# Kernel optimization log

Hardware: AMD Instinct MI355X
Metric: run time of the kernel (lower is better)

The kernel has to match this reference:

```python
import jax, jax.numpy as jnp
import numpy as np
from jax import lax

NSITE, NCELL, BSZ = 101, 64, 1
D_MODEL, D_INNER, D_STATE, D_CONV, DT_RANK = 64, 128, 16, 4, 4
L = NSITE * NCELL


def setup_inputs() -> dict:
    key = jax.random.key(0)
    ks = jax.random.split(key, 16)
    f = lambda k, s, sc=0.05: jax.random.normal(k, s, jnp.float32) * sc
    return {
        "DNAinput": f(ks[0], (BSZ, L, 32), 1.0),
        "CpGinput": f(ks[1], (BSZ, L, 16), 1.0),
        "cellinput": f(ks[2], (BSZ, L, 16), 1.0),
        "pos": f(ks[3], (BSZ, L, D_MODEL), 1.0),
        "y_true": jax.random.uniform(ks[4], (64,), jnp.float32),
        "W_fcc": f(ks[5], (64, D_MODEL)),
        "b_fcc": jnp.zeros((D_MODEL,), jnp.float32),
        "W_in": f(ks[6], (D_MODEL, 2 * D_INNER)),
        "conv_w": f(ks[7], (D_INNER, D_CONV)),
        "conv_b": jnp.zeros((D_INNER,), jnp.float32),
        "W_xp": f(ks[8], (D_INNER, DT_RANK + 2 * D_STATE)),
        "W_dt": f(ks[9], (DT_RANK, D_INNER)),
        "b_dt": f(ks[10], (D_INNER,)),
        "A_log": jnp.log(jnp.broadcast_to(jnp.arange(1, D_STATE + 1, dtype=jnp.float32), (D_INNER, D_STATE))),
        "Dres": jnp.ones((D_INNER,), jnp.float32),
        "W_out": f(ks[11], (D_INNER, D_MODEL)),
        "ln_g": jnp.ones((D_MODEL,), jnp.float32),
        "ln_b": jnp.zeros((D_MODEL,), jnp.float32),
        "W_fc": f(ks[12], (D_MODEL, 1)),
        "b_fc": jnp.zeros((1,), jnp.float32),
        "halfwin": 50,
        "row_index_s": jax.random.randint(ks[13], (64,), 0, NCELL),
    }


def _silu(x):
    return x * jax.nn.sigmoid(x)


def _layernorm(x, g, b, eps=1e-5):
    m = jnp.mean(x, -1, keepdims=True)
    v = jnp.var(x, -1, keepdims=True)
    return (x - m) * lax.rsqrt(v + eps) * g + b


def _mamba(x, W_in, conv_w, conv_b, W_xp, W_dt, b_dt, A_log, Dres, W_out):
    # x: (B, L, d_model)
    xz = x @ W_in                                   # (B, L, 2*d_inner)
    xi, z = jnp.split(xz, 2, axis=-1)
    # depthwise causal conv1d, kernel D_CONV
    xt = xi.transpose(0, 2, 1)                      # (B, d_inner, L)
    xc = lax.conv_general_dilated(
        xt, conv_w[:, None, :], (1,), [(D_CONV - 1, 0)],
        feature_group_count=D_INNER, dimension_numbers=("NCH", "OIH", "NCH"))
    xc = _silu((xc + conv_b[None, :, None]).transpose(0, 2, 1))  # (B, L, d_inner)
    xdbl = xc @ W_xp                                # (B, L, dt_rank + 2*d_state)
    dt = jax.nn.softplus(xdbl[..., :DT_RANK] @ W_dt + b_dt)      # (B, L, d_inner)
    Bm = xdbl[..., DT_RANK:DT_RANK + D_STATE]       # (B, L, d_state)
    Cm = xdbl[..., DT_RANK + D_STATE:]              # (B, L, d_state)
    A = -jnp.exp(A_log)                             # (d_inner, d_state)
    a_bar = jnp.exp(dt[..., None] * A)              # (B, L, d_inner, d_state)
    b_bar = (dt * xc)[..., None] * Bm[..., None, :]

    def comb(e1, e2):
        a1, b1 = e1
        a2, b2 = e2
        return a1 * a2, a2 * b1 + b2

    _, h = lax.associative_scan(comb, (a_bar, b_bar), axis=1)    # h_t = a_t h_{t-1} + b_t
    y = jnp.einsum("blds,bls->bld", h, Cm) + xc * Dres
    return (y * _silu(z)) @ W_out


def reference(DNAinput, CpGinput, cellinput, pos, y_true, W_fcc, b_fcc, W_in, conv_w, conv_b, W_xp, W_dt, b_dt, A_log, Dres, W_out, ln_g, ln_b, W_fc, b_fc, halfwin, row_index_s):
    x = jnp.concatenate((CpGinput, cellinput, DNAinput), -1) + pos
    x = (x @ W_fcc + b_fcc).reshape(BSZ, -1, D_MODEL)
    mb = lambda u: _mamba(u, W_in, conv_w, conv_b, W_xp, W_dt, b_dt, A_log, Dres, W_out)
    for _ in range(4):
        x = _layernorm(x + (mb(x) + jnp.flip(mb(jnp.flip(x, 1)), 1)) / 2, ln_g, ln_b)
        x = x.reshape(BSZ, NSITE, NCELL, D_MODEL).transpose(0, 2, 1, 3).reshape(BSZ, -1, D_MODEL)
        x = _layernorm(x + (mb(x) + jnp.flip(mb(jnp.flip(x, 1)), 1)) / 2, ln_g, ln_b)
        x = x.reshape(BSZ, NCELL, NSITE, D_MODEL).transpose(0, 2, 1, 3).reshape(BSZ, -1, D_MODEL)
    y_hat = (x.reshape(BSZ, NSITE, NCELL, D_MODEL) @ W_fc + b_fc)[..., 0]  # (B, nsite, ncell)
    y_sel = y_hat[0, halfwin, row_index_s].reshape(-1)
    return 1.0 - jnp.abs(y_true - jax.nn.sigmoid(y_sel))
```

## Files before the change

kernel.cpp:

```cpp
#include <hip/hip_runtime.h>
#include <math.h>

#define L_SEQ 6464
#define DM 64
#define DI 128
#define DS 16
#define CHUNK 101
#define NCH 64

__global__ void k_embed(const float* __restrict__ DNA, const float* __restrict__ CpG,
                        const float* __restrict__ cell, const float* __restrict__ pos,
                        const float* __restrict__ Wfcc, const float* __restrict__ bfcc,
                        float* __restrict__ x0) {
    int l = blockIdx.x;
    int j = threadIdx.x;
    __shared__ float in64[64];
    float v;
    if (j < 16)       v = CpG[l * 16 + j];
    else if (j < 32)  v = cell[l * 16 + (j - 16)];
    else              v = DNA[l * 32 + (j - 32)];
    v += pos[l * 64 + j];
    in64[j] = v;
    __syncthreads();
    float acc = bfcc[j];
    for (int i = 0; i < 64; i++) acc += in64[i] * Wfcc[i * 64 + j];
    x0[(size_t)l * 64 + j] = acc;
}

__global__ void __launch_bounds__(256) k_gemm_in(const float* __restrict__ x,
                                                 const float* __restrict__ Win,
                                                 float* __restrict__ xz) {
    __shared__ float s_x[8][64];
    int t0 = blockIdx.x * 8;
    int tid = threadIdx.x;
    for (int i = tid; i < 8 * 64; i += 256) {
        int rr = i >> 6, c = i & 63;
        s_x[rr][c] = x[(size_t)(t0 + rr) * 64 + c];
    }
    __syncthreads();
    int j = tid;
    float acc[8];
    #pragma unroll
    for (int r = 0; r < 8; r++) acc[r] = 0.f;
    for (int i = 0; i < 64; i++) {
        float w = Win[i * 256 + j];
        #pragma unroll
        for (int r = 0; r < 8; r++) acc[r] = fmaf(s_x[r][i], w, acc[r]);
    }
    #pragma unroll
    for (int r = 0; r < 8; r++) xz[(size_t)(t0 + r) * 256 + j] = acc[r];
}

__global__ void __launch_bounds__(256) k_convdt(
        const float* __restrict__ xz, const float* __restrict__ convw,
        const float* __restrict__ convb, const float* __restrict__ Wxp,
        const float* __restrict__ Wdt, const float* __restrict__ bdt,
        float* __restrict__ xc, float* __restrict__ dt, float* __restrict__ BC) {
    __shared__ __align__(16) float s_xi[22][128];
    __shared__ __align__(16) float s_xc[16][128];
    __shared__ float s_xd[16][36];
    __shared__ __align__(16) float s_wxpT[36][132];
    int t0 = blockIdx.x * 16;
    int tid = threadIdx.x;
    for (int i = tid; i < 36 * 128; i += 256) {
        int ii = i / 36, t = i - ii * 36;
        s_wxpT[t][ii] = Wxp[i];
    }
    for (int i = tid; i < 22 * 32; i += 256) {
        int rr = i >> 5, q = i & 31;
        int r = t0 - 3 + rr;
        float4 v = make_float4(0.f, 0.f, 0.f, 0.f);
        if (r >= 0 && r < L_SEQ) v = *(const float4*)&xz[(size_t)r * 256 + 4 * q];
        s_xi[rr][4 * q + 0] = v.x;
        s_xi[rr][4 * q + 1] = v.y;
        s_xi[rr][4 * q + 2] = v.z;
        s_xi[rr][4 * q + 3] = v.w;
    }
    __syncthreads();
    for (int dir = 0; dir < 2; dir++) {
        for (int i = tid; i < 16 * 128; i += 256) {
            int rr = i >> 7, d = i & 127;
            int lr = rr + 3;
            float acc = convb[d];
            if (dir == 0) {
                #pragma unroll
                for (int k = 0; k < 4; k++) acc += convw[d * 4 + k] * s_xi[lr - 3 + k][d];
            } else {
                #pragma unroll
                for (int k = 0; k < 4; k++) acc += convw[d * 4 + k] * s_xi[lr + 3 - k][d];
            }
            float v = acc / (1.f + expf(-acc));
            s_xc[rr][d] = v;
            xc[((size_t)dir * L_SEQ + t0 + rr) * 128 + d] = v;
        }
        __syncthreads();
        for (int o = tid; o < 16 * 36; o += 256) {
            int rr = o / 36, t = o % 36;
            float acc = 0.f;
            #pragma unroll 8
            for (int i = 0; i < 128; i += 4) {
                const float4 xv = *(const float4*)&s_xc[rr][i];
                const float4 wv = *(const float4*)&s_wxpT[t][i];
                acc = fmaf(xv.x, wv.x, acc);
                acc = fmaf(xv.y, wv.y, acc);
                acc = fmaf(xv.z, wv.z, acc);
                acc = fmaf(xv.w, wv.w, acc);
            }
            s_xd[rr][t] = acc;
        }
        __syncthreads();
        for (int o = tid; o < 16 * 128; o += 256) {
            int rr = o >> 7, d = o & 127;
            float pre = bdt[d];
            #pragma unroll
            for (int r = 0; r < 4; r++) pre += s_xd[rr][r] * Wdt[r * 128 + d];
            float dtv = (pre > 20.f) ? pre : log1pf(expf(pre));
            dt[((size_t)dir * L_SEQ + t0 + rr) * 128 + d] = dtv;
        }
        for (int o = tid; o < 16 * 32; o += 256) {
            int rr = o >> 5, w = o & 31;
            BC[((size_t)dir * L_SEQ + t0 + rr) * 32 + w] = s_xd[rr][4 + w];
        }
        __syncthreads();
    }
}

__global__ void __launch_bounds__(256) k_scanA(
        const float* __restrict__ dt, const float* __restrict__ xc,
        const float* __restrict__ BC, const float* __restrict__ Alog,
        float* __restrict__ cA, float* __restrict__ cB) {
    __shared__ __align__(16) float s_dt[CHUNK * 32];
    __shared__ __align__(16) float s_xc[CHUNK * 32];
    __shared__ __align__(16) float s_b [CHUNK * 16];
    int g    = blockIdx.x;
    int c    = blockIdx.y;
    int dir  = blockIdx.z;
    int tid  = threadIdx.x;
    int dl = tid >> 3, sp = tid & 7;
    int d = g * 32 + dl;
    const float* dtp = dt + (size_t)dir * L_SEQ * DI;
    const float* xcp = xc + (size_t)dir * L_SEQ * DI;
    const float* bcp = BC + (size_t)dir * L_SEQ * 32;
    int t0 = c * CHUNK;
    int slab0 = dir ? (L_SEQ - CHUNK - t0) : t0;
    for (int i = tid; i < CHUNK * 8; i += 256) {
        int ro = i >> 3, q = i & 7;
        int row = slab0 + ro;
        int tl = dir ? (CHUNK - 1 - ro) : ro;
        *(float4*)&s_dt[tl * 32 + 4 * q] = *(const float4*)&dtp[(size_t)row * DI + g * 32 + 4 * q];
        *(float4*)&s_xc[tl * 32 + 4 * q] = *(const float4*)&xcp[(size_t)row * DI + g * 32 + 4 * q];
    }
    for (int i = tid; i < CHUNK * 4; i += 256) {
        int ro = i >> 2, q = i & 3;
        int row = slab0 + ro;
        int tl = dir ? (CHUNK - 1 - ro) : ro;
        *(float4*)&s_b[tl * 16 + 4 * q] = *(const float4*)&bcp[(size_t)row * 32 + 4 * q];
    }
    float A0 = -expf(Alog[d * 16 + 2 * sp]);
    float A1 = -expf(Alog[d * 16 + 2 * sp + 1]);
    __syncthreads();
    float h0 = 0.f, h1 = 0.f, ap0 = 1.f, ap1 = 1.f;
    #pragma unroll 4
    for (int tl = 0; tl < CHUNK; tl++) {
        float dv = s_dt[tl * 32 + dl];
        float xv = s_xc[tl * 32 + dl];
        float t1 = dv * xv;
        float2 bq = *(const float2*)&s_b[tl * 16 + 2 * sp];
        float a0 = __expf(dv * A0); h0 = fmaf(a0, h0, t1 * bq.x); ap0 *= a0;
        float a1 = __expf(dv * A1); h1 = fmaf(a1, h1, t1 * bq.y); ap1 *= a1;
    }
    size_t o0 = (size_t)dir * 131072 + (size_t)c * 2048 + (size_t)(2 * sp) * 128 + d;
    size_t o1 = o0 + 128;
    cA[o0] = ap0; cB[o0] = h0;
    cA[o1] = ap1; cB[o1] = h1;
}

__global__ void __launch_bounds__(256) k_fold(const float* __restrict__ cA,
                                              const float* __restrict__ cB,
                                              float* __restrict__ F) {
    int idx = blockIdx.x * 256 + threadIdx.x;
    int dir = idx >> 11;
    int rem = idx & 2047;
    int s = rem >> 7;
    int d = rem & 127;
    size_t o = (size_t)dir * 131072 + (size_t)s * 128 + d;
    float carry = 0.f;
    for (int cc = 0; cc < NCH; cc += 8) {
        float av[8], bv[8];
        #pragma unroll
        for (int j = 0; j < 8; j++) {
            size_t oo = o + (size_t)(cc + j) * 2048;
            av[j] = cA[oo];
            bv[j] = cB[oo];
        }
        #pragma unroll
        for (int j = 0; j < 8; j++) {
            F[o + (size_t)(cc + j) * 2048] = carry;
            carry = fmaf(av[j], carry, bv[j]);
        }
    }
}

__global__ void __launch_bounds__(256) k_scanB(
        const float* __restrict__ dt, const float* __restrict__ xc,
        const float* __restrict__ BC, const float* __restrict__ Alog,
        const float* __restrict__ Dres, const float* __restrict__ F,
        float* __restrict__ y) {
    __shared__ __align__(16) float s_dt[CHUNK * 32];
    __shared__ __align__(16) float s_xc[CHUNK * 32];
    __shared__ __align__(16) float s_bc[CHUNK * 32];
    int g    = blockIdx.x;
    int c    = blockIdx.y;
    int dir  = blockIdx.z;
    int tid  = threadIdx.x;
    int dl = tid >> 3, sp = tid & 7;
    int d = g * 32 + dl;
    const float* dtp = dt + (size_t)dir * L_SEQ * DI;
    const float* xcp = xc + (size_t)dir * L_SEQ * DI;
    const float* bcp = BC + (size_t)dir * L_SEQ * 32;
    float* yp = y + (size_t)dir * L_SEQ * DI;
    int t0 = c * CHUNK;
    int slab0 = dir ? (L_SEQ - CHUNK - t0) : t0;
    for (int i = tid; i < CHUNK * 8; i += 256) {
        int ro = i >> 3, q = i & 7;
        int row = slab0 + ro;
        int tl = dir ? (CHUNK - 1 - ro) : ro;
        *(float4*)&s_dt[tl * 32 + 4 * q] = *(const float4*)&dtp[(size_t)row * DI + g * 32 + 4 * q];
        *(float4*)&s_xc[tl * 32 + 4 * q] = *(const float4*)&xcp[(size_t)row * DI + g * 32 + 4 * q];
        *(float4*)&s_bc[tl * 32 + 4 * q] = *(const float4*)&bcp[(size_t)row * 32 + 4 * q];
    }
    float A0 = -expf(Alog[d * 16 + 2 * sp]);
    float A1 = -expf(Alog[d * 16 + 2 * sp + 1]);
    size_t o0 = (size_t)dir * 131072 + (size_t)c * 2048 + (size_t)(2 * sp) * 128 + d;
    float h0 = F[o0];
    float h1 = F[o0 + 128];
    float Dv = Dres[d];
    __syncthreads();
    #pragma unroll 4
    for (int tl = 0; tl < CHUNK; tl++) {
        float dv = s_dt[tl * 32 + dl];
        float xv = s_xc[tl * 32 + dl];
        float t1 = dv * xv;
        float2 bq = *(const float2*)&s_bc[tl * 32 + 2 * sp];
        float2 cq = *(const float2*)&s_bc[tl * 32 + 16 + 2 * sp];
        float a0 = __expf(dv * A0); h0 = fmaf(a0, h0, t1 * bq.x);
        float a1 = __expf(dv * A1); h1 = fmaf(a1, h1, t1 * bq.y);
        float p0 = h0 * cq.x, p1 = h1 * cq.y;
        float qv = p0 + p1;
        float rv = qv + __shfl_xor(qv, 1);
        float uv = rv + __shfl_xor(rv, 2);
        float val = uv + __shfl_xor(uv, 4);
        if (sp == 0) s_dt[tl * 32 + dl] = val + xv * Dv;
    }
    __syncthreads();
    for (int i = tid; i < CHUNK * 8; i += 256) {
        int ro = i >> 3, q = i & 7;
        int row = slab0 + ro;
        int tl = dir ? (CHUNK - 1 - ro) : ro;
        float4 v = *(const float4*)&s_dt[tl * 32 + 4 * q];
        *(float4*)&yp[(size_t)row * DI + g * 32 + 4 * q] = v;
    }
}

__global__ void __launch_bounds__(256) k_outln(
        const float* __restrict__ x, const float* __restrict__ y,
        const float* __restrict__ xz, const float* __restrict__ Wout,
        const float* __restrict__ Win, const float* __restrict__ lng,
        const float* __restrict__ lnb, float* __restrict__ xnext,
        float* __restrict__ xznext, int permMode, int doXz) {
    __shared__ float s_g[4][128];
    __shared__ float s_out[4][64];
    __shared__ int s_l2[4];
    int tid = threadIdx.x;
    int w = tid >> 6;
    int j = tid & 63;
    int l = blockIdx.x * 4 + w;
    float z1 = xz[(size_t)l * 256 + 128 + j];
    float z2 = xz[(size_t)l * 256 + 192 + j];
    float sz1 = z1 / (1.f + expf(-z1));
    float sz2 = z2 / (1.f + expf(-z2));
    s_g[w][j]      = 0.5f * (y[(size_t)l * 128 + j] + y[(size_t)(L_SEQ + l) * 128 + j]) * sz1;
    s_g[w][j + 64] = 0.5f * (y[(size_t)l * 128 + 64 + j] + y[(size_t)(L_SEQ + l) * 128 + 64 + j]) * sz2;
    __syncthreads();
    float acc = x[(size_t)l * 64 + j];
    for (int i = 0; i < 128; i++) acc += s_g[w][i] * Wout[i * 64 + j];
    float m = acc;
    for (int o = 32; o >= 1; o >>= 1) m += __shfl_xor(m, o);
    m *= (1.f / 64.f);
    float dv = acc - m;
    float v = dv * dv;
    for (int o = 32; o >= 1; o >>= 1) v += __shfl_xor(v, o);
    v *= (1.f / 64.f);
    float out = dv * rsqrtf(v + 1e-5f) * lng[j] + lnb[j];
    int l2;
    if (permMode == 0) l2 = (l % 64) * 101 + (l / 64);
    else               l2 = (l % 101) * 64 + (l / 101);
    xnext[(size_t)l2 * 64 + j] = out;
    if (!doXz) return;
    s_out[w][j] = out;
    if (j == 0) s_l2[w] = l2;
    __syncthreads();
    float xa[4];
    #pragma unroll
    for (int r = 0; r < 4; r++) xa[r] = 0.f;
    for (int i = 0; i < 64; i++) {
        float wv = Win[i * 256 + tid];
        #pragma unroll
        for (int r = 0; r < 4; r++) xa[r] = fmaf(s_out[r][i], wv, xa[r]);
    }
    #pragma unroll
    for (int r = 0; r < 4; r++) xznext[(size_t)s_l2[r] * 256 + tid] = xa[r];
}

__global__ void k_epilogue(const float* __restrict__ x, const float* __restrict__ Wfc,
                           const float* __restrict__ bfc, const float* __restrict__ ytrue,
                           const int* __restrict__ halfwin, const int* __restrict__ rows,
                           float* __restrict__ out) {
    int k = threadIdx.x;
    int hw = halfwin[0];
    int c = rows[k];
    const float* xr = x + ((size_t)hw * 64 + c) * 64;
    float acc = bfc[0];
    for (int i = 0; i < 64; i++) acc += xr[i] * Wfc[i];
    float s = 1.f / (1.f + expf(-acc));
    float r = 1.f - fabsf(ytrue[k] - s);
    out[k] = r;
}

extern "C" void kernel_launch(void* const* d_in, const int* in_sizes, int n_in,
                              void* d_out, int out_size, void* d_ws, size_t ws_size,
                              hipStream_t stream) {
    const float* DNA   = (const float*)d_in[0];
    const float* CpG   = (const float*)d_in[1];
    const float* cel   = (const float*)d_in[2];
    const float* pos   = (const float*)d_in[3];
    const float* ytrue = (const float*)d_in[4];
    const float* Wfcc  = (const float*)d_in[5];
    const float* bfcc  = (const float*)d_in[6];
    const float* Win   = (const float*)d_in[7];
    const float* convw = (const float*)d_in[8];
    const float* convb = (const float*)d_in[9];
    const float* Wxp   = (const float*)d_in[10];
    const float* Wdt   = (const float*)d_in[11];
    const float* bdt   = (const float*)d_in[12];
    const float* Alog  = (const float*)d_in[13];
    const float* Dres  = (const float*)d_in[14];
    const float* Wout  = (const float*)d_in[15];
    const float* lng   = (const float*)d_in[16];
    const float* lnb   = (const float*)d_in[17];
    const float* Wfc   = (const float*)d_in[18];
    const float* bfc   = (const float*)d_in[19];
    const int* halfwin = (const int*)d_in[20];
    const int* rows    = (const int*)d_in[21];

    float* ws = (float*)d_ws;
    size_t off = 0;
    float* x0  = ws + off; off += (size_t)L_SEQ * 64;
    float* x1  = ws + off; off += (size_t)L_SEQ * 64;
    float* xzA = ws + off; off += (size_t)L_SEQ * 256;
    float* xzB = ws + off; off += (size_t)L_SEQ * 256;
    float* xcb = ws + off; off += (size_t)2 * L_SEQ * 128;
    float* dtb = ws + off; off += (size_t)2 * L_SEQ * 128;
    float* BCb = ws + off; off += (size_t)2 * L_SEQ * 32;
    float* yb  = ws + off; off += (size_t)2 * L_SEQ * 128;
    float* cAb = ws + off; off += (size_t)2 * NCH * 2048;
    float* cBb = ws + off; off += (size_t)2 * NCH * 2048;
    float* Fb  = ws + off; off += (size_t)2 * NCH * 2048;

    k_embed<<<L_SEQ, 64, 0, stream>>>(DNA, CpG, cel, pos, Wfcc, bfcc, x0);

    float* xcur = x0;
    float* xnxt = x1;
    float* xzc  = xzA;
    float* xzn  = xzB;
    k_gemm_in<<<L_SEQ / 8, 256, 0, stream>>>(xcur, Win, xzc);
    for (int sb = 0; sb < 8; sb++) {
        k_convdt<<<L_SEQ / 16, 256, 0, stream>>>(xzc, convw, convb, Wxp, Wdt, bdt, xcb, dtb, BCb);
        k_scanA<<<dim3(4, NCH, 2), 256, 0, stream>>>(dtb, xcb, BCb, Alog, cAb, cBb);
        k_fold<<<16, 256, 0, stream>>>(cAb, cBb, Fb);
        k_scanB<<<dim3(4, NCH, 2), 256, 0, stream>>>(dtb, xcb, BCb, Alog, Dres, Fb, yb);
        k_outln<<<L_SEQ / 4, 256, 0, stream>>>(xcur, yb, xzc, Wout, Win, lng, lnb, xnxt, xzn,
                                               (sb % 2 == 0) ? 0 : 1, (sb < 7) ? 1 : 0);
        float* tmp = xcur; xcur = xnxt; xnxt = tmp;
        float* tz = xzc; xzc = xzn; xzn = tz;
    }

    k_epilogue<<<1, 64, 0, stream>>>(xcur, Wfc, bfc, ytrue, halfwin, rows, (float*)d_out);
}
```

Baseline: 736.2 us.

## Fold chunk carries inside scanB and batch 16 rows per outln block

Drops the separate k_fold launch. Each k_scanB thread now recomputes its incoming carry by serially folding the (A, B) chunk summaries of all earlier chunks before running its own chunk. k_outln now handles 16 rows per block instead of 4, so each Wout and Win weight load is reused across more rows. The risk is redundant and unbalanced carry work in scanB, since later chunks fold up to 63 summaries, plus higher register pressure from the 16-wide accumulator in outln.

```diff
diff --git a/kernel.cpp b/kernel.cpp
--- a/kernel.cpp
+++ b/kernel.cpp
@@ -175,37 +175,11 @@
     cA[o1] = ap1; cB[o1] = h1;
 }
 
-__global__ void __launch_bounds__(256) k_fold(const float* __restrict__ cA,
-                                              const float* __restrict__ cB,
-                                              float* __restrict__ F) {
-    int idx = blockIdx.x * 256 + threadIdx.x;
-    int dir = idx >> 11;
-    int rem = idx & 2047;
-    int s = rem >> 7;
-    int d = rem & 127;
-    size_t o = (size_t)dir * 131072 + (size_t)s * 128 + d;
-    float carry = 0.f;
-    for (int cc = 0; cc < NCH; cc += 8) {
-        float av[8], bv[8];
-        #pragma unroll
-        for (int j = 0; j < 8; j++) {
-            size_t oo = o + (size_t)(cc + j) * 2048;
-            av[j] = cA[oo];
-            bv[j] = cB[oo];
-        }
-        #pragma unroll
-        for (int j = 0; j < 8; j++) {
-            F[o + (size_t)(cc + j) * 2048] = carry;
-            carry = fmaf(av[j], carry, bv[j]);
-        }
-    }
-}
-
 __global__ void __launch_bounds__(256) k_scanB(
         const float* __restrict__ dt, const float* __restrict__ xc,
         const float* __restrict__ BC, const float* __restrict__ Alog,
-        const float* __restrict__ Dres, const float* __restrict__ F,
-        float* __restrict__ y) {
+        const float* __restrict__ Dres, const float* __restrict__ cA,
+        const float* __restrict__ cB, float* __restrict__ y) {
     __shared__ __align__(16) float s_dt[CHUNK * 32];
     __shared__ __align__(16) float s_xc[CHUNK * 32];
     __shared__ __align__(16) float s_bc[CHUNK * 32];
@@ -229,11 +203,27 @@
         *(float4*)&s_xc[tl * 32 + 4 * q] = *(const float4*)&xcp[(size_t)row * DI + g * 32 + 4 * q];
         *(float4*)&s_bc[tl * 32 + 4 * q] = *(const float4*)&bcp[(size_t)row * 32 + 4 * q];
     }
+    float h0 = 0.f, h1 = 0.f;
+    {
+        size_t base0 = (size_t)dir * 131072 + (size_t)(2 * sp) * 128 + d;
+        int cc = 0;
+        while (cc < c) {
+            int n = (c - cc < 8) ? (c - cc) : 8;
+            float a0v[8], b0v[8], a1v[8], b1v[8];
+            for (int jj = 0; jj < n; jj++) {
+                size_t oo = base0 + (size_t)(cc + jj) * 2048;
+                a0v[jj] = cA[oo];       b0v[jj] = cB[oo];
+                a1v[jj] = cA[oo + 128]; b1v[jj] = cB[oo + 128];
+            }
+            for (int jj = 0; jj < n; jj++) {
+                h0 = fmaf(a0v[jj], h0, b0v[jj]);
+                h1 = fmaf(a1v[jj], h1, b1v[jj]);
+            }
+            cc += n;
+        }
+    }
     float A0 = -expf(Alog[d * 16 + 2 * sp]);
     float A1 = -expf(Alog[d * 16 + 2 * sp + 1]);
-    size_t o0 = (size_t)dir * 131072 + (size_t)c * 2048 + (size_t)(2 * sp) * 128 + d;
-    float h0 = F[o0];
-    float h1 = F[o0 + 128];
     float Dv = Dres[d];
     __syncthreads();
     #pragma unroll 4
@@ -268,48 +258,62 @@
         const float* __restrict__ Win, const float* __restrict__ lng,
         const float* __restrict__ lnb, float* __restrict__ xnext,
         float* __restrict__ xznext, int permMode, int doXz) {
-    __shared__ float s_g[4][128];
-    __shared__ float s_out[4][64];
-    __shared__ int s_l2[4];
+    __shared__ float s_g[16][128];
+    __shared__ float s_out[16][64];
+    __shared__ int s_l2[16];
     int tid = threadIdx.x;
-    int w = tid >> 6;
-    int j = tid & 63;
-    int l = blockIdx.x * 4 + w;
-    float z1 = xz[(size_t)l * 256 + 128 + j];
-    float z2 = xz[(size_t)l * 256 + 192 + j];
-    float sz1 = z1 / (1.f + expf(-z1));
-    float sz2 = z2 / (1.f + expf(-z2));
-    s_g[w][j]      = 0.5f * (y[(size_t)l * 128 + j] + y[(size_t)(L_SEQ + l) * 128 + j]) * sz1;
-    s_g[w][j + 64] = 0.5f * (y[(size_t)l * 128 + 64 + j] + y[(size_t)(L_SEQ + l) * 128 + 64 + j]) * sz2;
-    __syncthreads();
-    float acc = x[(size_t)l * 64 + j];
-    for (int i = 0; i < 128; i++) acc += s_g[w][i] * Wout[i * 64 + j];
-    float m = acc;
-    for (int o = 32; o >= 1; o >>= 1) m += __shfl_xor(m, o);
-    m *= (1.f / 64.f);
-    float dv = acc - m;
-    float v = dv * dv;
-    for (int o = 32; o >= 1; o >>= 1) v += __shfl_xor(v, o);
-    v *= (1.f / 64.f);
-    float out = dv * rsqrtf(v + 1e-5f) * lng[j] + lnb[j];
-    int l2;
-    if (permMode == 0) l2 = (l % 64) * 101 + (l / 64);
-    else               l2 = (l % 101) * 64 + (l / 101);
-    xnext[(size_t)l2 * 64 + j] = out;
+    int l0 = blockIdx.x * 16;
+    for (int e = tid; e < 16 * 128; e += 256) {
+        int r = e >> 7, k = e & 127;
+        int l = l0 + r;
+        float z = xz[(size_t)l * 256 + 128 + k];
+        float sz = z / (1.f + expf(-z));
+        s_g[r][k] = 0.5f * (y[(size_t)l * 128 + k] + y[(size_t)(L_SEQ + l) * 128 + k]) * sz;
+    }
+    if (tid < 16) {
+        int l = l0 + tid;
+        int l2;
+        if (permMode == 0) l2 = (l % 64) * 101 + (l / 64);
+        else               l2 = (l % 101) * 64 + (l / 101);
+        s_l2[tid] = l2;
+    }
+    __syncthreads();
+    int w = tid >> 6, j = tid & 63;
+    float acc[4];
+    #pragma unroll
+    for (int k = 0; k < 4; k++) acc[k] = x[(size_t)(l0 + w + 4 * k) * 64 + j];
+    for (int i = 0; i < 128; i++) {
+        float wv = Wout[i * 64 + j];
+        #pragma unroll
+        for (int k = 0; k < 4; k++) acc[k] = fmaf(s_g[w + 4 * k][i], wv, acc[k]);
+    }
+    #pragma unroll
+    for (int k = 0; k < 4; k++) {
+        float a = acc[k];
+        float m = a;
+        for (int o = 32; o >= 1; o >>= 1) m += __shfl_xor(m, o);
+        m *= (1.f / 64.f);
+        float dv = a - m;
+        float v = dv * dv;
+        for (int o = 32; o >= 1; o >>= 1) v += __shfl_xor(v, o);
+        v *= (1.f / 64.f);
+        float out = dv * rsqrtf(v + 1e-5f) * lng[j] + lnb[j];
+        int r = w + 4 * k;
+        xnext[(size_t)s_l2[r] * 64 + j] = out;
+        s_out[r][j] = out;
+    }
     if (!doXz) return;
-    s_out[w][j] = out;
-    if (j == 0) s_l2[w] = l2;
-    __syncthreads();
-    float xa[4];
-    #pragma unroll
-    for (int r = 0; r < 4; r++) xa[r] = 0.f;
+    __syncthreads();
+    float xa[16];
+    #pragma unroll
+    for (int r = 0; r < 16; r++) xa[r] = 0.f;
     for (int i = 0; i < 64; i++) {
         float wv = Win[i * 256 + tid];
         #pragma unroll
-        for (int r = 0; r < 4; r++) xa[r] = fmaf(s_out[r][i], wv, xa[r]);
-    }
-    #pragma unroll
-    for (int r = 0; r < 4; r++) xznext[(size_t)s_l2[r] * 256 + tid] = xa[r];
+        for (int r = 0; r < 16; r++) xa[r] = fmaf(s_out[r][i], wv, xa[r]);
+    }
+    #pragma unroll
+    for (int r = 0; r < 16; r++) xznext[(size_t)s_l2[r] * 256 + tid] = xa[r];
 }
 
 __global__ void k_epilogue(const float* __restrict__ x, const float* __restrict__ Wfc,
@@ -365,7 +369,6 @@
     float* yb  = ws + off; off += (size_t)2 * L_SEQ * 128;
     float* cAb = ws + off; off += (size_t)2 * NCH * 2048;
     float* cBb = ws + off; off += (size_t)2 * NCH * 2048;
-    float* Fb  = ws + off; off += (size_t)2 * NCH * 2048;
 
     k_embed<<<L_SEQ, 64, 0, stream>>>(DNA, CpG, cel, pos, Wfcc, bfcc, x0);
 
@@ -377,10 +380,9 @@
     for (int sb = 0; sb < 8; sb++) {
         k_convdt<<<L_SEQ / 16, 256, 0, stream>>>(xzc, convw, convb, Wxp, Wdt, bdt, xcb, dtb, BCb);
         k_scanA<<<dim3(4, NCH, 2), 256, 0, stream>>>(dtb, xcb, BCb, Alog, cAb, cBb);
-        k_fold<<<16, 256, 0, stream>>>(cAb, cBb, Fb);
-        k_scanB<<<dim3(4, NCH, 2), 256, 0, stream>>>(dtb, xcb, BCb, Alog, Dres, Fb, yb);
-        k_outln<<<L_SEQ / 4, 256, 0, stream>>>(xcur, yb, xzc, Wout, Win, lng, lnb, xnxt, xzn,
-                                               (sb % 2 == 0) ? 0 : 1, (sb < 7) ? 1 : 0);
+        k_scanB<<<dim3(4, NCH, 2), 256, 0, stream>>>(dtb, xcb, BCb, Alog, Dres, cAb, cBb, yb);
+        k_outln<<<L_SEQ / 16, 256, 0, stream>>>(xcur, yb, xzc, Wout, Win, lng, lnb, xnxt, xzn,
+                                                (sb % 2 == 0) ? 0 : 1, (sb < 7) ? 1 : 0);
         float* tmp = xcur; xcur = xnxt; xnxt = tmp;
         float* tz = xzc; xzc = xzn; xzn = tz;
     }
```

Result: slower. 965.2 us (+31.1%).

## Split scanB chunk into two halves using mid-chunk partial states from scanA

Applied to the files above, without the earlier changes.

scanA now also stores the partial scan state at the chunk midpoint (step 51). scanB runs with 512 threads, and the second half of the threads starts from the carry combined with that midpoint state, so each half scans about 50 steps instead of 101. This shortens the serial recurrence in scanB. In exchange it adds extra global writes and reads for the midpoint state and needs twice as many threads per block.

```diff
diff --git a/kernel.cpp b/kernel.cpp
--- a/kernel.cpp
+++ b/kernel.cpp
@@ -128,7 +128,8 @@
 __global__ void __launch_bounds__(256) k_scanA(
         const float* __restrict__ dt, const float* __restrict__ xc,
         const float* __restrict__ BC, const float* __restrict__ Alog,
-        float* __restrict__ cA, float* __restrict__ cB) {
+        float* __restrict__ cA, float* __restrict__ cB,
+        float* __restrict__ cAm, float* __restrict__ cBm) {
     __shared__ __align__(16) float s_dt[CHUNK * 32];
     __shared__ __align__(16) float s_xc[CHUNK * 32];
     __shared__ __align__(16) float s_b [CHUNK * 16];
@@ -160,8 +161,10 @@
     float A1 = -expf(Alog[d * 16 + 2 * sp + 1]);
     __syncthreads();
     float h0 = 0.f, h1 = 0.f, ap0 = 1.f, ap1 = 1.f;
+    size_t o0 = (size_t)dir * 131072 + (size_t)c * 2048 + (size_t)(2 * sp) * 128 + d;
+    int tl = 0;
     #pragma unroll 4
-    for (int tl = 0; tl < CHUNK; tl++) {
+    for (; tl < 51; tl++) {
         float dv = s_dt[tl * 32 + dl];
         float xv = s_xc[tl * 32 + dl];
         float t1 = dv * xv;
@@ -169,10 +172,19 @@
         float a0 = __expf(dv * A0); h0 = fmaf(a0, h0, t1 * bq.x); ap0 *= a0;
         float a1 = __expf(dv * A1); h1 = fmaf(a1, h1, t1 * bq.y); ap1 *= a1;
     }
-    size_t o0 = (size_t)dir * 131072 + (size_t)c * 2048 + (size_t)(2 * sp) * 128 + d;
-    size_t o1 = o0 + 128;
+    cAm[o0] = ap0; cBm[o0] = h0;
+    cAm[o0 + 128] = ap1; cBm[o0 + 128] = h1;
+    #pragma unroll 4
+    for (; tl < CHUNK; tl++) {
+        float dv = s_dt[tl * 32 + dl];
+        float xv = s_xc[tl * 32 + dl];
+        float t1 = dv * xv;
+        float2 bq = *(const float2*)&s_b[tl * 16 + 2 * sp];
+        float a0 = __expf(dv * A0); h0 = fmaf(a0, h0, t1 * bq.x); ap0 *= a0;
+        float a1 = __expf(dv * A1); h1 = fmaf(a1, h1, t1 * bq.y); ap1 *= a1;
+    }
     cA[o0] = ap0; cB[o0] = h0;
-    cA[o1] = ap1; cB[o1] = h1;
+    cA[o0 + 128] = ap1; cB[o0 + 128] = h1;
 }
 
 __global__ void __launch_bounds__(256) k_fold(const float* __restrict__ cA,
@@ -201,10 +213,11 @@
     }
 }
 
-__global__ void __launch_bounds__(256) k_scanB(
+__global__ void __launch_bounds__(512) k_scanB(
         const float* __restrict__ dt, const float* __restrict__ xc,
         const float* __restrict__ BC, const float* __restrict__ Alog,
         const float* __restrict__ Dres, const float* __restrict__ F,
+        const float* __restrict__ cAm, const float* __restrict__ cBm,
         float* __restrict__ y) {
     __shared__ __align__(16) float s_dt[CHUNK * 32];
     __shared__ __align__(16) float s_xc[CHUNK * 32];
@@ -213,7 +226,9 @@
     int c    = blockIdx.y;
     int dir  = blockIdx.z;
     int tid  = threadIdx.x;
-    int dl = tid >> 3, sp = tid & 7;
+    int half = tid >> 8;
+    int t8 = tid & 255;
+    int dl = t8 >> 3, sp = t8 & 7;
     int d = g * 32 + dl;
     const float* dtp = dt + (size_t)dir * L_SEQ * DI;
     const float* xcp = xc + (size_t)dir * L_SEQ * DI;
@@ -221,7 +236,7 @@
     float* yp = y + (size_t)dir * L_SEQ * DI;
     int t0 = c * CHUNK;
     int slab0 = dir ? (L_SEQ - CHUNK - t0) : t0;
-    for (int i = tid; i < CHUNK * 8; i += 256) {
+    for (int i = tid; i < CHUNK * 8; i += 512) {
         int ro = i >> 3, q = i & 7;
         int row = slab0 + ro;
         int tl = dir ? (CHUNK - 1 - ro) : ro;
@@ -234,10 +249,18 @@
     size_t o0 = (size_t)dir * 131072 + (size_t)c * 2048 + (size_t)(2 * sp) * 128 + d;
     float h0 = F[o0];
     float h1 = F[o0 + 128];
+    if (half) {
+        float am0 = cAm[o0], bm0 = cBm[o0];
+        float am1 = cAm[o0 + 128], bm1 = cBm[o0 + 128];
+        h0 = fmaf(am0, h0, bm0);
+        h1 = fmaf(am1, h1, bm1);
+    }
     float Dv = Dres[d];
     __syncthreads();
+    int tl0 = half ? 51 : 0;
+    int tl1 = half ? CHUNK : 51;
     #pragma unroll 4
-    for (int tl = 0; tl < CHUNK; tl++) {
+    for (int tl = tl0; tl < tl1; tl++) {
         float dv = s_dt[tl * 32 + dl];
         float xv = s_xc[tl * 32 + dl];
         float t1 = dv * xv;
@@ -253,7 +276,7 @@
         if (sp == 0) s_dt[tl * 32 + dl] = val + xv * Dv;
     }
     __syncthreads();
-    for (int i = tid; i < CHUNK * 8; i += 256) {
+    for (int i = tid; i < CHUNK * 8; i += 512) {
         int ro = i >> 3, q = i & 7;
         int row = slab0 + ro;
         int tl = dir ? (CHUNK - 1 - ro) : ro;
@@ -366,6 +389,8 @@
     float* cAb = ws + off; off += (size_t)2 * NCH * 2048;
     float* cBb = ws + off; off += (size_t)2 * NCH * 2048;
     float* Fb  = ws + off; off += (size_t)2 * NCH * 2048;
+    float* cAm = ws + off; off += (size_t)2 * NCH * 2048;
+    float* cBm = ws + off; off += (size_t)2 * NCH * 2048;
 
     k_embed<<<L_SEQ, 64, 0, stream>>>(DNA, CpG, cel, pos, Wfcc, bfcc, x0);
 
@@ -376,9 +401,9 @@
     k_gemm_in<<<L_SEQ / 8, 256, 0, stream>>>(xcur, Win, xzc);
     for (int sb = 0; sb < 8; sb++) {
         k_convdt<<<L_SEQ / 16, 256, 0, stream>>>(xzc, convw, convb, Wxp, Wdt, bdt, xcb, dtb, BCb);
-        k_scanA<<<dim3(4, NCH, 2), 256, 0, stream>>>(dtb, xcb, BCb, Alog, cAb, cBb);
+        k_scanA<<<dim3(4, NCH, 2), 256, 0, stream>>>(dtb, xcb, BCb, Alog, cAb, cBb, cAm, cBm);
         k_fold<<<16, 256, 0, stream>>>(cAb, cBb, Fb);
-        k_scanB<<<dim3(4, NCH, 2), 256, 0, stream>>>(dtb, xcb, BCb, Alog, Dres, Fb, yb);
+        k_scanB<<<dim3(4, NCH, 2), 512, 0, stream>>>(dtb, xcb, BCb, Alog, Dres, Fb, cAm, cBm, yb);
         k_outln<<<L_SEQ / 4, 256, 0, stream>>>(xcur, yb, xzc, Wout, Win, lng, lnb, xnxt, xzn,
                                                (sb % 2 == 0) ? 0 : 1, (sb < 7) ? 1 : 0);
         float* tmp = xcur; xcur = xnxt; xnxt = tmp;
```

Result: faster. 698.3 us (-5.1%).

## Split scanB chunk into four sub-segments using scanA mid-chunk checkpoints

Applied to the files above, without the earlier changes.

scanA now writes intermediate (cumulative decay, state) checkpoints at three points inside each 101-step chunk. scanB launches 1024 threads per block, with four 256-thread groups that each rebuild their starting state from the chunk carry and a checkpoint, then scan about 25 steps instead of 101. This shortens the serial dependency chain in scanB by about four times and raises parallelism from 512 blocks of 256 threads. The cost is extra global writes and reads of checkpoint data, a larger workspace, and a 1024-thread block that may limit registers per thread and occupancy.

```diff
diff --git a/kernel.cpp b/kernel.cpp
--- a/kernel.cpp
+++ b/kernel.cpp
@@ -7,6 +7,7 @@
 #define DS 16
 #define CHUNK 101
 #define NCH 64
+#define CSZ 262144
 
 __global__ void k_embed(const float* __restrict__ DNA, const float* __restrict__ CpG,
                         const float* __restrict__ cell, const float* __restrict__ pos,
@@ -128,7 +129,8 @@
 __global__ void __launch_bounds__(256) k_scanA(
         const float* __restrict__ dt, const float* __restrict__ xc,
         const float* __restrict__ BC, const float* __restrict__ Alog,
-        float* __restrict__ cA, float* __restrict__ cB) {
+        float* __restrict__ cA, float* __restrict__ cB,
+        float* __restrict__ cAm, float* __restrict__ cBm) {
     __shared__ __align__(16) float s_dt[CHUNK * 32];
     __shared__ __align__(16) float s_xc[CHUNK * 32];
     __shared__ __align__(16) float s_b [CHUNK * 16];
@@ -160,19 +162,30 @@
     float A1 = -expf(Alog[d * 16 + 2 * sp + 1]);
     __syncthreads();
     float h0 = 0.f, h1 = 0.f, ap0 = 1.f, ap1 = 1.f;
-    #pragma unroll 4
-    for (int tl = 0; tl < CHUNK; tl++) {
-        float dv = s_dt[tl * 32 + dl];
-        float xv = s_xc[tl * 32 + dl];
-        float t1 = dv * xv;
-        float2 bq = *(const float2*)&s_b[tl * 16 + 2 * sp];
-        float a0 = __expf(dv * A0); h0 = fmaf(a0, h0, t1 * bq.x); ap0 *= a0;
-        float a1 = __expf(dv * A1); h1 = fmaf(a1, h1, t1 * bq.y); ap1 *= a1;
-    }
     size_t o0 = (size_t)dir * 131072 + (size_t)c * 2048 + (size_t)(2 * sp) * 128 + d;
-    size_t o1 = o0 + 128;
+    int tl = 0;
+#define ASTEP { \
+        float dv = s_dt[tl * 32 + dl]; \
+        float xv = s_xc[tl * 32 + dl]; \
+        float t1 = dv * xv; \
+        float2 bq = *(const float2*)&s_b[tl * 16 + 2 * sp]; \
+        float a0 = __expf(dv * A0); h0 = fmaf(a0, h0, t1 * bq.x); ap0 *= a0; \
+        float a1 = __expf(dv * A1); h1 = fmaf(a1, h1, t1 * bq.y); ap1 *= a1; }
+    #pragma unroll 2
+    for (; tl < 26; tl++) ASTEP
+    cAm[o0] = ap0; cBm[o0] = h0; cAm[o0 + 128] = ap1; cBm[o0 + 128] = h1;
+    #pragma unroll 2
+    for (; tl < 51; tl++) ASTEP
+    cAm[CSZ + o0] = ap0; cBm[CSZ + o0] = h0; cAm[CSZ + o0 + 128] = ap1; cBm[CSZ + o0 + 128] = h1;
+    #pragma unroll 2
+    for (; tl < 76; tl++) ASTEP
+    cAm[2 * CSZ + o0] = ap0; cBm[2 * CSZ + o0] = h0;
+    cAm[2 * CSZ + o0 + 128] = ap1; cBm[2 * CSZ + o0 + 128] = h1;
+    #pragma unroll 2
+    for (; tl < CHUNK; tl++) ASTEP
+#undef ASTEP
     cA[o0] = ap0; cB[o0] = h0;
-    cA[o1] = ap1; cB[o1] = h1;
+    cA[o0 + 128] = ap1; cB[o0 + 128] = h1;
 }
 
 __global__ void __launch_bounds__(256) k_fold(const float* __restrict__ cA,
@@ -201,10 +214,11 @@
     }
 }
 
-__global__ void __launch_bounds__(256) k_scanB(
+__global__ void __launch_bounds__(1024) k_scanB(
         const float* __restrict__ dt, const float* __restrict__ xc,
         const float* __restrict__ BC, const float* __restrict__ Alog,
         const float* __restrict__ Dres, const float* __restrict__ F,
+        const float* __restrict__ cAm, const float* __restrict__ cBm,
         float* __restrict__ y) {
     __shared__ __align__(16) float s_dt[CHUNK * 32];
     __shared__ __align__(16) float s_xc[CHUNK * 32];
@@ -213,7 +227,9 @@
     int c    = blockIdx.y;
     int dir  = blockIdx.z;
     int tid  = threadIdx.x;
-    int dl = tid >> 3, sp = tid & 7;
+    int seg  = tid >> 8;
+    int t8 = tid & 255;
+    int dl = t8 >> 3, sp = t8 & 7;
     int d = g * 32 + dl;
     const float* dtp = dt + (size_t)dir * L_SEQ * DI;
     const float* xcp = xc + (size_t)dir * L_SEQ * DI;
@@ -221,7 +237,7 @@
     float* yp = y + (size_t)dir * L_SEQ * DI;
     int t0 = c * CHUNK;
     int slab0 = dir ? (L_SEQ - CHUNK - t0) : t0;
-    for (int i = tid; i < CHUNK * 8; i += 256) {
+    for (int i = tid; i < CHUNK * 8; i += 1024) {
         int ro = i >> 3, q = i & 7;
         int row = slab0 + ro;
         int tl = dir ? (CHUNK - 1 - ro) : ro;
@@ -234,10 +250,17 @@
     size_t o0 = (size_t)dir * 131072 + (size_t)c * 2048 + (size_t)(2 * sp) * 128 + d;
     float h0 = F[o0];
     float h1 = F[o0 + 128];
+    if (seg) {
+        size_t mo = (size_t)(seg - 1) * CSZ + o0;
+        h0 = fmaf(cAm[mo], h0, cBm[mo]);
+        h1 = fmaf(cAm[mo + 128], h1, cBm[mo + 128]);
+    }
     float Dv = Dres[d];
     __syncthreads();
+    int tl0 = (seg == 0) ? 0 : (26 + 25 * (seg - 1));
+    int tl1 = (seg == 0) ? 26 : (tl0 + 25);
     #pragma unroll 4
-    for (int tl = 0; tl < CHUNK; tl++) {
+    for (int tl = tl0; tl < tl1; tl++) {
         float dv = s_dt[tl * 32 + dl];
         float xv = s_xc[tl * 32 + dl];
         float t1 = dv * xv;
@@ -253,7 +276,7 @@
         if (sp == 0) s_dt[tl * 32 + dl] = val + xv * Dv;
     }
     __syncthreads();
-    for (int i = tid; i < CHUNK * 8; i += 256) {
+    for (int i = tid; i < CHUNK * 8; i += 1024) {
         int ro = i >> 3, q = i & 7;
         int row = slab0 + ro;
         int tl = dir ? (CHUNK - 1 - ro) : ro;
@@ -363,9 +386,11 @@
     float* dtb = ws + off; off += (size_t)2 * L_SEQ * 128;
     float* BCb = ws + off; off += (size_t)2 * L_SEQ * 32;
     float* yb  = ws + off; off += (size_t)2 * L_SEQ * 128;
-    float* cAb = ws + off; off += (size_t)2 * NCH * 2048;
-    float* cBb = ws + off; off += (size_t)2 * NCH * 2048;
-    float* Fb  = ws + off; off += (size_t)2 * NCH * 2048;
+    float* cAb = ws + off; off += (size_t)CSZ;
+    float* cBb = ws + off; off += (size_t)CSZ;
+    float* Fb  = ws + off; off += (size_t)CSZ;
+    float* cAm = ws + off; off += (size_t)3 * CSZ;
+    float* cBm = ws + off; off += (size_t)3 * CSZ;
 
     k_embed<<<L_SEQ, 64, 0, stream>>>(DNA, CpG, cel, pos, Wfcc, bfcc, x0);
 
@@ -376,9 +401,9 @@
     k_gemm_in<<<L_SEQ / 8, 256, 0, stream>>>(xcur, Win, xzc);
     for (int sb = 0; sb < 8; sb++) {
         k_convdt<<<L_SEQ / 16, 256, 0, stream>>>(xzc, convw, convb, Wxp, Wdt, bdt, xcb, dtb, BCb);
-        k_scanA<<<dim3(4, NCH, 2), 256, 0, stream>>>(dtb, xcb, BCb, Alog, cAb, cBb);
+        k_scanA<<<dim3(4, NCH, 2), 256, 0, stream>>>(dtb, xcb, BCb, Alog, cAb, cBb, cAm, cBm);
         k_fold<<<16, 256, 0, stream>>>(cAb, cBb, Fb);
-        k_scanB<<<dim3(4, NCH, 2), 256, 0, stream>>>(dtb, xcb, BCb, Alog, Dres, Fb, yb);
+        k_scanB<<<dim3(4, NCH, 2), 1024, 0, stream>>>(dtb, xcb, BCb, Alog, Dres, Fb, cAm, cBm, yb);
         k_outln<<<L_SEQ / 4, 256, 0, stream>>>(xcur, yb, xzc, Wout, Win, lng, lnb, xnxt, xzn,
                                                (sb % 2 == 0) ? 0 : 1, (sb < 7) ? 1 : 0);
         float* tmp = xcur; xcur = xnxt; xnxt = tmp;
```

New measurement: 710.4 us. -3.5%, faster.
